# Kernel tuning notes

Hardware: AMD Instinct MI355X
Metric: run time of the kernel (lower is better)

Reference implementation:

```python
import jax, jax.numpy as jnp
import numpy as np

MAX_NORM = 2.0  # Lorentz(max_norm=2.0)


def expmap0(u):
    # geoopt-style Lorentz expmap0 (k=1) with tangent max-norm clipping and
    # final projection back onto the hyperboloid (project=True).
    en = jnp.linalg.norm(u, axis=-1, keepdims=True)
    u = u * jnp.minimum(1.0, MAX_NORM / jnp.maximum(en, 1e-12))
    inner = -u[..., :1] ** 2 + jnp.sum(u[..., 1:] ** 2, axis=-1, keepdims=True)
    nomin = jnp.sqrt(jnp.maximum(inner, 1e-8))
    r_v = jnp.sinh(nomin) * u / nomin
    p = jnp.concatenate([jnp.cosh(nomin) + r_v[..., :1], r_v[..., 1:]], axis=-1)
    space = p[..., 1:]
    time = jnp.sqrt(1.0 + jnp.sum(space ** 2, axis=-1, keepdims=True))
    return jnp.concatenate([time, space], axis=-1)


def householder_product(vv):
    # vv: (B, W, d) gelu'd rows of the relation rotation matrix; product of
    # W Householder reflections H_w = I - 2 v v^T / ||v||^2, accumulated
    # left-to-right: P = H_0 @ H_1 @ ... @ H_{W-1} (same math as the
    # original Python loop, applied as rank-1 updates via lax.scan).
    B, W, d = vv.shape
    norms = jnp.sum(vv * vv, axis=-1)  # (B, W) -- original has no eps here
    P0 = jnp.broadcast_to(jnp.eye(d, dtype=vv.dtype), (B, d, d))

    def step(P, vn):
        v, n = vn  # (B, d), (B,)
        Pv = jnp.einsum('bij,bj->bi', P, v)
        return P - 2.0 * Pv[:, :, None] * v[:, None, :] / n[:, None, None], None

    P, _ = jax.lax.scan(step, P0, (jnp.moveaxis(vv, 1, 0), jnp.moveaxis(norms, 1, 0)))
    return P  # (B, d, d)


def setup_inputs() -> dict:
    key = jax.random.key(0)
    n_ent, n_rel, rank, B = 50000, 500, 33, 2000
    k1, k2, k3, k4, k5, k6 = jax.random.split(key, 6)
    ent = jax.random.normal(k1, (n_ent, rank), jnp.float32) * 0.01
    rot = jax.random.normal(k2, (n_rel, rank - 1, rank - 1), jnp.float32) * 0.1
    boosts = jax.random.normal(k3, (n_rel, rank - 1), jnp.float32) * 0.1
    heads = jax.random.randint(k4, (B,), 0, n_ent)
    rels = jax.random.randint(k5, (B,), 0, n_rel)
    tails = jax.random.randint(k6, (B,), 0, n_ent)
    queries = jnp.stack([heads, rels, tails], axis=1).astype(jnp.int64)
    return {'ent_embeddings': ent, 'rel_rotate': rot, 'rel_boosts': boosts,
            'queries': queries}


def reference(ent_embeddings, rel_rotate, rel_boosts, queries):
    rank = ent_embeddings.shape[-1]
    emb = expmap0(ent_embeddings)                       # (N, rank) on hyperboloid
    lhs = emb[queries[:, 0]]                            # (B, rank)
    rot = jax.nn.gelu(rel_rotate[queries[:, 1]], approximate=False)  # (B, d, d)
    b_raw = rel_boosts[queries[:, 1]]                   # (B, d)

    lhs_t, lhs_s = lhs[:, :1], lhs[:, 1:]
    # lorentz_rotate
    P = householder_product(rot)
    lhs_s = jnp.einsum('bi,bij->bj', lhs_s, P)
    # lorentz_boosts
    b = jnp.tanh(b_raw) / rank
    b2 = jnp.sum(b * b, axis=-1, keepdims=True)
    zeta = 1.0 / (jnp.sqrt(1.0 - b2) + 1e-8)
    bdot = jnp.sum(b * lhs_s, axis=-1, keepdims=True)
    x0 = zeta * lhs_t - zeta * bdot
    xr = -zeta * lhs_t * b + lhs_s + (zeta - 1.0) / (b2 + 1e-9) * b * bdot
    lhs2 = jnp.concatenate([x0, xr], axis=-1)           # (B, rank)

    # cinner: Lorentzian inner product against all entities
    lhs_neg = jnp.concatenate([-lhs2[:, :1], lhs2[:, 1:]], axis=-1)
    scores = 2.0 - 2.0 * (lhs_neg @ emb.T)              # (B, N)
    # eval mode: reg_noise is zeros -> no-op

    reg = (jnp.sqrt(jnp.sum(rel_rotate.reshape(rel_rotate.shape[0], -1) ** 2, axis=-1))
           + jnp.sqrt(jnp.sum(rel_boosts ** 2, axis=-1, keepdims=True)))  # broadcasts to (n_rel, n_rel) as in torch
    return scores, reg
```

## Files before the change

kernel.cpp:

```cpp
#include <hip/hip_runtime.h>
#include <math.h>

#define RANK 33
#define D 32
#define N_ENT 50000
#define N_REL 500
#define NQ 2000
#define W_PAD 50176
#define NQ_PAD 2048
#define MT 100

typedef float f2v __attribute__((ext_vector_type(2)));

__device__ __forceinline__ float waveReduceSum(float v) {
    #pragma unroll
    for (int off = 32; off > 0; off >>= 1)
        v += __shfl_xor(v, off, 64);
    return v;
}

__global__ void k_expmap(const float* __restrict__ ent, float* __restrict__ embT) {
    int wave = (blockIdx.x * blockDim.x + threadIdx.x) >> 6;
    int lane = threadIdx.x & 63;
    if (wave >= N_ENT) return;
    const float* u = ent + (long)wave * RANK;
    float uv = (lane < RANK) ? u[lane] : 0.0f;
    float en = sqrtf(waveReduceSum(uv * uv));
    float scale = fminf(1.0f, 2.0f / fmaxf(en, 1e-12f));
    uv *= scale;
    float sp2 = waveReduceSum((lane >= 1 && lane < RANK) ? uv * uv : 0.0f);
    float u0 = __shfl(uv, 0, 64);
    float inner = sp2 - u0 * u0;
    float nomin = sqrtf(fmaxf(inner, 1e-8f));
    float s = sinhf(nomin) / nomin;
    float sv = s * uv;
    float t2 = waveReduceSum((lane >= 1 && lane < RANK) ? sv * sv : 0.0f);
    if (lane == 0) embT[wave] = sqrtf(1.0f + t2);
    if (lane >= 1 && lane < RANK) embT[(size_t)lane * W_PAD + wave] = sv;
}

__global__ void k_query(const float* __restrict__ embT,
                        const float* __restrict__ rot_raw,
                        const float* __restrict__ boosts,
                        const int* __restrict__ queries,
                        float* __restrict__ lhsT) {
    int wave = (blockIdx.x * blockDim.x + threadIdx.x) >> 6;
    int lane = threadIdx.x & 63;
    if (wave >= NQ) return;
    int h = queries[wave * 3 + 0];
    int r = queries[wave * 3 + 1];
    float lhs_t = embT[h];
    float x = (lane < D) ? embT[(size_t)(1 + lane) * W_PAD + h] : 0.0f;
    const float* rr = rot_raw + (long)r * D * D;
    for (int k = 0; k < D; ++k) {
        float g = 0.0f;
        if (lane < D) {
            float w = rr[k * D + lane];
            g = 0.5f * w * (1.0f + erff(w * 0.70710678118654752f));
        }
        float dvx = waveReduceSum(g * x);
        float n   = waveReduceSum(g * g);
        x -= (2.0f * dvx / n) * g;
    }
    float b = 0.0f;
    if (lane < D) b = tanhf(boosts[(long)r * D + lane]) * (1.0f / 33.0f);
    float b2   = waveReduceSum(b * b);
    float bdot = waveReduceSum(b * x);
    float zeta = 1.0f / (sqrtf(1.0f - b2) + 1e-8f);
    float x0 = zeta * lhs_t - zeta * bdot;
    float xr = -zeta * lhs_t * b + x + (zeta - 1.0f) / (b2 + 1e-9f) * b * bdot;
    if (lane < D) lhsT[(size_t)(1 + lane) * NQ_PAD + wave] = xr;
    if (lane == 0) lhsT[wave] = -x0;
}

__global__ void k_scores(const float* __restrict__ lhsT,
                         const float* __restrict__ embT,
                         float* __restrict__ out) {
    int t = threadIdx.x;
    int n = blockIdx.x * 512 + t * 2;
    if (n >= N_ENT) return;
    int m0 = blockIdx.y * MT;
    f2v e[RANK];
    #pragma unroll
    for (int k = 0; k < RANK; ++k)
        e[k] = *(const f2v*)(embT + (size_t)k * W_PAD + n);
    for (int mt = m0; mt < m0 + MT; mt += 4) {
        float a0x = 0.f, a0y = 0.f, a1x = 0.f, a1y = 0.f;
        float a2x = 0.f, a2y = 0.f, a3x = 0.f, a3y = 0.f;
        #pragma unroll
        for (int k = 0; k < RANK; ++k) {
            float4 l = *(const float4*)(lhsT + k * NQ_PAD + mt);
            float ex = e[k].x, ey = e[k].y;
            a0x = fmaf(l.x, ex, a0x); a0y = fmaf(l.x, ey, a0y);
            a1x = fmaf(l.y, ex, a1x); a1y = fmaf(l.y, ey, a1y);
            a2x = fmaf(l.z, ex, a2x); a2y = fmaf(l.z, ey, a2y);
            a3x = fmaf(l.w, ex, a3x); a3y = fmaf(l.w, ey, a3y);
        }
        f2v s0 = {2.f - 2.f * a0x, 2.f - 2.f * a0y};
        f2v s1 = {2.f - 2.f * a1x, 2.f - 2.f * a1y};
        f2v s2 = {2.f - 2.f * a2x, 2.f - 2.f * a2y};
        f2v s3 = {2.f - 2.f * a3x, 2.f - 2.f * a3y};
        __builtin_nontemporal_store(s0, (f2v*)(out + (size_t)(mt + 0) * N_ENT + n));
        __builtin_nontemporal_store(s1, (f2v*)(out + (size_t)(mt + 1) * N_ENT + n));
        __builtin_nontemporal_store(s2, (f2v*)(out + (size_t)(mt + 2) * N_ENT + n));
        __builtin_nontemporal_store(s3, (f2v*)(out + (size_t)(mt + 3) * N_ENT + n));
    }
}

__global__ void k_norms(const float* __restrict__ rot_raw,
                        const float* __restrict__ boosts,
                        float* __restrict__ rotF, float* __restrict__ boostN) {
    int wave = (blockIdx.x * blockDim.x + threadIdx.x) >> 6;
    int lane = threadIdx.x & 63;
    if (wave >= N_REL) return;
    const float* rr = rot_raw + (long)wave * (D * D);
    float s = 0.0f;
    #pragma unroll
    for (int i = 0; i < (D * D) / 64; ++i) {
        float w = rr[i * 64 + lane];
        s += w * w;
    }
    s = waveReduceSum(s);
    float sb = 0.0f;
    if (lane < D) { float w = boosts[(long)wave * D + lane]; sb = w * w; }
    sb = waveReduceSum(sb);
    if (lane == 0) { rotF[wave] = sqrtf(s); boostN[wave] = sqrtf(sb); }
}

__global__ void k_reg(const float* __restrict__ rotF, const float* __restrict__ boostN,
                      float* __restrict__ out) {
    int idx = blockIdx.x * blockDim.x + threadIdx.x;
    if (idx >= N_REL * N_REL) return;
    int i = idx / N_REL;
    int j = idx - i * N_REL;
    out[idx] = rotF[j] + boostN[i];
}

extern "C" void kernel_launch(void* const* d_in, const int* in_sizes, int n_in,
                              void* d_out, int out_size, void* d_ws, size_t ws_size,
                              hipStream_t stream) {
    const float* ent     = (const float*)d_in[0];
    const float* rot     = (const float*)d_in[1];
    const float* boosts  = (const float*)d_in[2];
    const int*   queries = (const int*)d_in[3];
    float* out = (float*)d_out;

    float* ws     = (float*)d_ws;
    float* embT   = ws;
    float* lhsT   = ws + (size_t)RANK * W_PAD;
    float* rotF   = lhsT + (size_t)RANK * NQ_PAD;
    float* boostN = rotF + N_REL;

    hipLaunchKernelGGL(k_expmap, dim3((N_ENT + 3) / 4), dim3(256), 0, stream, ent, embT);
    hipLaunchKernelGGL(k_query, dim3(NQ / 4), dim3(256), 0, stream,
                       embT, rot, boosts, queries, lhsT);
    hipLaunchKernelGGL(k_scores, dim3(98, NQ / MT), dim3(256), 0, stream,
                       lhsT, embT, out);
    hipLaunchKernelGGL(k_norms, dim3((N_REL + 3) / 4), dim3(256), 0, stream,
                       rot, boosts, rotF, boostN);
    hipLaunchKernelGGL(k_reg, dim3((N_REL * N_REL + 255) / 256), dim3(256), 0, stream,
                       rotF, boostN, out + (size_t)NQ * N_ENT);
}
```

Measured before the change: 147.1 us.

## Compute expmap per-thread and recompute head embeddings in query kernel

```diff
diff --git a/kernel.cpp b/kernel.cpp
--- a/kernel.cpp
+++ b/kernel.cpp
@@ -20,26 +20,31 @@
 }
 
 __global__ void k_expmap(const float* __restrict__ ent, float* __restrict__ embT) {
-    int wave = (blockIdx.x * blockDim.x + threadIdx.x) >> 6;
-    int lane = threadIdx.x & 63;
-    if (wave >= N_ENT) return;
-    const float* u = ent + (long)wave * RANK;
-    float uv = (lane < RANK) ? u[lane] : 0.0f;
-    float en = sqrtf(waveReduceSum(uv * uv));
-    float scale = fminf(1.0f, 2.0f / fmaxf(en, 1e-12f));
-    uv *= scale;
-    float sp2 = waveReduceSum((lane >= 1 && lane < RANK) ? uv * uv : 0.0f);
-    float u0 = __shfl(uv, 0, 64);
-    float inner = sp2 - u0 * u0;
-    float nomin = sqrtf(fmaxf(inner, 1e-8f));
+    int n = blockIdx.x * blockDim.x + threadIdx.x;
+    if (n >= N_ENT) return;
+    const float* u = ent + (size_t)n * RANK;
+    float v[RANK];
+    float en2 = 0.f;
+    #pragma unroll
+    for (int k = 0; k < RANK; ++k) { v[k] = u[k]; en2 += v[k] * v[k]; }
+    float scale = fminf(1.0f, 2.0f / fmaxf(sqrtf(en2), 1e-12f));
+    #pragma unroll
+    for (int k = 0; k < RANK; ++k) v[k] *= scale;
+    float sp2 = 0.f;
+    #pragma unroll
+    for (int k = 1; k < RANK; ++k) sp2 += v[k] * v[k];
+    float nomin = sqrtf(fmaxf(sp2 - v[0] * v[0], 1e-8f));
     float s = sinhf(nomin) / nomin;
-    float sv = s * uv;
-    float t2 = waveReduceSum((lane >= 1 && lane < RANK) ? sv * sv : 0.0f);
-    if (lane == 0) embT[wave] = sqrtf(1.0f + t2);
-    if (lane >= 1 && lane < RANK) embT[(size_t)lane * W_PAD + wave] = sv;
+    float t2 = 0.f;
+    #pragma unroll
+    for (int k = 1; k < RANK; ++k) { v[k] *= s; t2 += v[k] * v[k]; }
+    embT[n] = sqrtf(1.0f + t2);
+    #pragma unroll
+    for (int k = 1; k < RANK; ++k)
+        embT[(size_t)k * W_PAD + n] = v[k];
 }
 
-__global__ void k_query(const float* __restrict__ embT,
+__global__ void k_query(const float* __restrict__ ent,
                         const float* __restrict__ rot_raw,
                         const float* __restrict__ boosts,
                         const int* __restrict__ queries,
@@ -49,8 +54,20 @@
     if (wave >= NQ) return;
     int h = queries[wave * 3 + 0];
     int r = queries[wave * 3 + 1];
-    float lhs_t = embT[h];
-    float x = (lane < D) ? embT[(size_t)(1 + lane) * W_PAD + h] : 0.0f;
+    const float* u = ent + (long)h * RANK;
+    float uv = (lane < RANK) ? u[lane] : 0.0f;
+    float en = sqrtf(waveReduceSum(uv * uv));
+    float scale = fminf(1.0f, 2.0f / fmaxf(en, 1e-12f));
+    uv *= scale;
+    float sp2 = waveReduceSum((lane >= 1 && lane < RANK) ? uv * uv : 0.0f);
+    float u0 = __shfl(uv, 0, 64);
+    float nomin = sqrtf(fmaxf(sp2 - u0 * u0, 1e-8f));
+    float s = sinhf(nomin) / nomin;
+    float sv = s * uv;
+    float t2 = waveReduceSum((lane >= 1 && lane < RANK) ? sv * sv : 0.0f);
+    float lhs_t = sqrtf(1.0f + t2);
+    float x = __shfl(sv, (lane + 1) & 63, 64);
+    if (lane >= D) x = 0.0f;
     const float* rr = rot_raw + (long)r * D * D;
     for (int k = 0; k < D; ++k) {
         float g = 0.0f;
@@ -151,9 +168,9 @@
     float* rotF   = lhsT + (size_t)RANK * NQ_PAD;
     float* boostN = rotF + N_REL;
 
-    hipLaunchKernelGGL(k_expmap, dim3((N_ENT + 3) / 4), dim3(256), 0, stream, ent, embT);
+    hipLaunchKernelGGL(k_expmap, dim3((N_ENT + 255) / 256), dim3(256), 0, stream, ent, embT);
     hipLaunchKernelGGL(k_query, dim3(NQ / 4), dim3(256), 0, stream,
-                       embT, rot, boosts, queries, lhsT);
+                       ent, rot, boosts, queries, lhsT);
     hipLaunchKernelGGL(k_scores, dim3(98, NQ / MT), dim3(256), 0, stream,
                        lhsT, embT, out);
     hipLaunchKernelGGL(k_norms, dim3((N_REL + 3) / 4), dim3(256), 0, stream,
```

New measurement: 136.4 us. 7.3% less time.
